# Kernel tuning notes

Measured on AMD Instinct MI355X. Metric: run time of the kernel, lower is better.

Reference implementation:

```python
import jax, jax.numpy as jnp
import numpy as np

B, S, H = 32, 2048, 1024

def setup_inputs() -> dict:
    key = jax.random.key(0)
    ks = jax.random.split(key, 8)
    scale = 1.0 / np.sqrt(H)
    return {
        "query": jax.random.normal(ks[0], (B, H), jnp.float32),
        "keys": jax.random.normal(ks[1], (B, S, H), jnp.float32),
        "Wa_w": jax.random.uniform(ks[2], (H, H), jnp.float32, -scale, scale),
        "Wa_b": jax.random.uniform(ks[3], (H,), jnp.float32, -scale, scale),
        "Ua_w": jax.random.uniform(ks[4], (H, H), jnp.float32, -scale, scale),
        "Ua_b": jax.random.uniform(ks[5], (H,), jnp.float32, -scale, scale),
        "Va_w": jax.random.uniform(ks[6], (1, H), jnp.float32, -scale, scale),
        "Va_b": jax.random.uniform(ks[7], (1,), jnp.float32, -scale, scale),
    }

def reference(query, keys, Wa_w, Wa_b, Ua_w, Ua_b, Va_w, Va_b):
    # q_proj: [B, H]; k_proj: [B, S, H]  (torch Linear: x @ W^T + b)
    q_proj = query @ Wa_w.T + Wa_b
    k_proj = jnp.einsum("bsh,gh->bsg", keys, Ua_w) + Ua_b
    # scores: [B, S, 1] via thin Va projection of tanh-combined features
    scores = jnp.tanh(q_proj[:, None, :] + k_proj) @ Va_w.T + Va_b
    weights = jax.nn.softmax(scores, axis=1)            # [B, S, 1]
    context = jnp.einsum("bsx,bsh->bxh", weights, keys)  # [B, 1, H]
    return context, weights[:, :, 0]
```

## Files before the change

### kernel.cpp

```cpp
#include <hip/hip_runtime.h>
#include <hip/hip_bf16.h>
#include <stdint.h>

#define B_ 32
#define S_ 2048
#define H_ 1024

typedef __attribute__((ext_vector_type(8))) short short8;
typedef __attribute__((ext_vector_type(4))) float floatx4;

__device__ inline unsigned short f32_bf16(float f) {
    union { float f; unsigned u; } v; v.f = f;
    unsigned u = v.u;
    u += 0x7fff + ((u >> 16) & 1);
    return (unsigned short)(u >> 16);
}
__device__ inline unsigned pack_bf2(float a, float b) {
    return (unsigned)f32_bf16(a) | ((unsigned)f32_bf16(b) << 16);
}
__device__ inline float bf_lo(unsigned u) { union { unsigned u; float f; } v; v.u = u << 16; return v.f; }
__device__ inline float bf_hi(unsigned u) { union { unsigned u; float f; } v; v.u = u & 0xffff0000u; return v.f; }

__device__ inline float tanh_fast(float x) {
    float e = __expf(2.0f * x);
    return 1.0f - 2.0f / (e + 1.0f);
}

__device__ inline void gld16(const void* g, void* l) {
    __builtin_amdgcn_global_load_lds(
        (const __attribute__((address_space(1))) unsigned int*)g,
        (__attribute__((address_space(3))) unsigned int*)l, 16, 0, 0);
}

#define KCVT_BLOCKS 32768
#define UACVT_BLOCKS 512
#define QP_BLOCKS 64
__global__ void k_prep(const float* __restrict__ keys, unsigned short* __restrict__ keysbf,
                       const float* __restrict__ ua, unsigned short* __restrict__ uab,
                       const float* __restrict__ query, const float* __restrict__ Wa_w,
                       const float* __restrict__ Wa_b, const float* __restrict__ Ua_b,
                       float* __restrict__ qsum) {
    int blk = blockIdx.x, t = threadIdx.x;
    if (blk < KCVT_BLOCKS + UACVT_BLOCKS) {
        const float* src; unsigned short* dst; size_t base;
        if (blk < KCVT_BLOCKS) { src = keys; dst = keysbf; base = (size_t)blk * 2048; }
        else { src = ua; dst = uab; base = (size_t)(blk - KCVT_BLOCKS) * 2048; }
        float4 v0 = *(const float4*)(src + base + t * 4);
        float4 v1 = *(const float4*)(src + base + 1024 + t * 4);
        *(uint2*)(dst + base + t * 4)        = make_uint2(pack_bf2(v0.x, v0.y), pack_bf2(v0.z, v0.w));
        *(uint2*)(dst + base + 1024 + t * 4) = make_uint2(pack_bf2(v1.x, v1.y), pack_bf2(v1.z, v1.w));
    } else {
        __shared__ float qs_l[32][68];
        int g0 = (blk - KCVT_BLOCKS - UACVT_BLOCKS) * 16;
        int r = t >> 4, l = t & 15;
        int g = g0 + r;
        float acc[32];
#pragma unroll
        for (int b = 0; b < 32; ++b) acc[b] = 0.0f;
        int sb = t >> 3, sc = (t & 7) * 8;
        for (int hc = 0; hc < 16; ++hc) {
            __syncthreads();
            float4 v0 = *(const float4*)(query + (size_t)sb * H_ + hc * 64 + sc);
            float4 v1 = *(const float4*)(query + (size_t)sb * H_ + hc * 64 + sc + 4);
            *(float4*)&qs_l[sb][sc]     = v0;
            *(float4*)&qs_l[sb][sc + 4] = v1;
            __syncthreads();
            float4 w = *(const float4*)(Wa_w + (size_t)g * H_ + hc * 64 + l * 4);
#pragma unroll
            for (int b = 0; b < 32; ++b) {
                float4 q4 = *(const float4*)&qs_l[b][l * 4];
                acc[b] += w.x * q4.x + w.y * q4.y + w.z * q4.z + w.w * q4.w;
            }
        }
#pragma unroll
        for (int b = 0; b < 32; ++b) {
            float a = acc[b];
            a += __shfl_xor(a, 1); a += __shfl_xor(a, 2);
            a += __shfl_xor(a, 4); a += __shfl_xor(a, 8);
            acc[b] = a;
        }
        if (l == 0) {
            float bias = Wa_b[g] + Ua_b[g];
#pragma unroll
            for (int b = 0; b < 32; ++b) qsum[b * H_ + g] = acc[b] + bias;
        }
    }
}

#define BM 128
#define BN 128
#define BK 64

__global__ __launch_bounds__(256, 4) void k_scores(
    const unsigned short* __restrict__ keysbf, const unsigned short* __restrict__ uab,
    const float* __restrict__ qsum, const float* __restrict__ va,
    float* __restrict__ scores_p)
{
    __shared__ unsigned short Al[BM * BK];
    __shared__ unsigned short Bl[BN * BK];

    int bx = blockIdx.x;
    int x  = bx & 7;
    int i  = bx >> 3;
    int tile_m = x * 64 + (i >> 3);
    int nc     = i & 7;
    int m_base = tile_m * BM;
    int b      = m_base >> 11;
    int g0     = nc * BN;

    int tid = threadIdx.x;
    int wid = tid >> 6, lane = tid & 63;
    int wm = wid >> 1, wn = wid & 1;
    int q = lane >> 4, cn = lane & 15;

    int rl8 = lane >> 3;
    int gcg = (lane & 7) ^ rl8;
    const unsigned short* pA[4];
    const unsigned short* pB[4];
    unsigned short* lA[4];
    unsigned short* lB[4];
#pragma unroll
    for (int j = 0; j < 4; ++j) {
        int row = wid * 32 + j * 8 + rl8;
        pA[j] = keysbf + (size_t)(m_base + row) * H_ + gcg * 8;
        pB[j] = uab    + (size_t)(g0     + row) * H_ + gcg * 8;
        lA[j] = &Al[(wid * 32 + j * 8) * BK];
        lB[j] = &Bl[(wid * 32 + j * 8) * BK];
    }

    int aoff[2][4], boff[2][4];
#pragma unroll
    for (int kk = 0; kk < 2; ++kk)
#pragma unroll
        for (int ii = 0; ii < 4; ++ii) {
            int r  = wm * 64 + ii * 16 + cn;
            aoff[kk][ii] = r * BK + ((kk * 4 + q) ^ (r & 7)) * 8;
            int rb = wn * 64 + ii * 16 + cn;
            boff[kk][ii] = rb * BK + ((kk * 4 + q) ^ (rb & 7)) * 8;
        }

    floatx4 acc[4][4];
#pragma unroll
    for (int ii = 0; ii < 4; ++ii)
#pragma unroll
        for (int jj = 0; jj < 4; ++jj)
            acc[ii][jj] = (floatx4)(0.0f);

    for (int kc = 0; kc < H_ / BK; ++kc) {
        __syncthreads();
        int ko = kc * BK;
#pragma unroll
        for (int j = 0; j < 4; ++j) {
            gld16(pA[j] + ko, lA[j]);
            gld16(pB[j] + ko, lB[j]);
        }
        __syncthreads();
#pragma unroll
        for (int kk = 0; kk < 2; ++kk) {
            short8 af[4], bf[4];
#pragma unroll
            for (int ii = 0; ii < 4; ++ii) af[ii] = *(const short8*)&Al[aoff[kk][ii]];
#pragma unroll
            for (int jj = 0; jj < 4; ++jj) bf[jj] = *(const short8*)&Bl[boff[kk][jj]];
#pragma unroll
            for (int ii = 0; ii < 4; ++ii)
#pragma unroll
                for (int jj = 0; jj < 4; ++jj)
                    acc[ii][jj] = __builtin_amdgcn_mfma_f32_16x16x32_bf16(
                        af[ii], bf[jj], acc[ii][jj], 0, 0, 0);
        }
    }

    float qs[4], vw[4];
#pragma unroll
    for (int jj = 0; jj < 4; ++jj) {
        int g = g0 + wn * 64 + jj * 16 + cn;
        qs[jj] = qsum[b * H_ + g];
        vw[jj] = va[g];
    }
    float* slab = scores_p + (size_t)nc * (B_ * S_) + b * S_;
#pragma unroll
    for (int ii = 0; ii < 4; ++ii) {
        float rs[4] = {0.f, 0.f, 0.f, 0.f};
#pragma unroll
        for (int jj = 0; jj < 4; ++jj) {
#pragma unroll
            for (int r = 0; r < 4; ++r)
                rs[r] += vw[jj] * tanh_fast(qs[jj] + acc[ii][jj][r]);
        }
#pragma unroll
        for (int r = 0; r < 4; ++r) {
            for (int mm = 1; mm < 16; mm <<= 1)
                rs[r] += __shfl_xor(rs[r], mm);
        }
        if (cn == 0) {
            int msrow = (m_base & (S_ - 1)) + wm * 64 + ii * 16 + q * 4;
            float* sp = slab + (size_t)wn * (8 * B_ * S_) + msrow;
            sp[0] = rs[0]; sp[1] = rs[1]; sp[2] = rs[2]; sp[3] = rs[3];
        }
    }
}

__global__ void k_softmax(const float* __restrict__ scores_p, float* __restrict__ weights) {
    int b = blockIdx.x;
    int t = threadIdx.x;
    __shared__ float red[4];
    float v[8];
    float mx = -1e30f;
#pragma unroll
    for (int k = 0; k < 8; ++k) {
        int idx = b * S_ + t + k * 256;
        float s = 0.0f;
#pragma unroll
        for (int p = 0; p < 16; ++p) s += scores_p[(size_t)p * (B_ * S_) + idx];
        v[k] = s; mx = fmaxf(mx, s);
    }
    for (int mm = 1; mm < 64; mm <<= 1) mx = fmaxf(mx, __shfl_xor(mx, mm));
    if ((t & 63) == 0) red[t >> 6] = mx;
    __syncthreads();
    mx = fmaxf(fmaxf(red[0], red[1]), fmaxf(red[2], red[3]));
    float sum = 0.0f;
#pragma unroll
    for (int k = 0; k < 8; ++k) { v[k] = __expf(v[k] - mx); sum += v[k]; }
    for (int mm = 1; mm < 64; mm <<= 1) sum += __shfl_xor(sum, mm);
    __syncthreads();
    if ((t & 63) == 0) red[t >> 6] = sum;
    __syncthreads();
    sum = red[0] + red[1] + red[2] + red[3];
    float inv = 1.0f / sum;
#pragma unroll
    for (int k = 0; k < 8; ++k) weights[b * S_ + t + k * 256] = v[k] * inv;
}

__global__ void k_ctx1(const unsigned short* __restrict__ keysbf,
                       const float* __restrict__ weights, float* __restrict__ partial) {
    int blk = blockIdx.x;
    int b = blk >> 5, sc = blk & 31;
    int t = threadIdx.x;
    __shared__ float wl[64];
    if (t < 64) wl[t] = weights[b * S_ + sc * 64 + t];
    __syncthreads();
    const uint4* kp = (const uint4*)(keysbf + (size_t)(b * S_ + sc * 64) * H_);
    int col = t & 127;
    int rp  = t >> 7;
    float a0=0,a1=0,a2=0,a3=0,a4=0,a5=0,a6=0,a7=0;
#pragma unroll 8
    for (int s = rp; s < 64; s += 2) {
        uint4 v = kp[(size_t)s * 128 + col];
        float w = wl[s];
        a0 += w * bf_lo(v.x); a1 += w * bf_hi(v.x);
        a2 += w * bf_lo(v.y); a3 += w * bf_hi(v.y);
        a4 += w * bf_lo(v.z); a5 += w * bf_hi(v.z);
        a6 += w * bf_lo(v.w); a7 += w * bf_hi(v.w);
    }
    float* pp = partial + (size_t)(b * 64 + sc * 2 + rp) * H_ + col * 8;
    float4 o0 = {a0, a1, a2, a3}, o1 = {a4, a5, a6, a7};
    *(float4*)pp = o0;
    *(float4*)(pp + 4) = o1;
}

__global__ void k_ctx2(const float* __restrict__ partial, float* __restrict__ ctx) {
    int b = blockIdx.x;
    int t = threadIdx.x;
    float4 a = {0.f, 0.f, 0.f, 0.f};
#pragma unroll 8
    for (int j = 0; j < 64; ++j) {
        float4 p = *(const float4*)(partial + (size_t)(b * 64 + j) * H_ + t * 4);
        a.x += p.x; a.y += p.y; a.z += p.z; a.w += p.w;
    }
    *(float4*)(ctx + b * H_ + t * 4) = a;
}

extern "C" void kernel_launch(void* const* d_in, const int* in_sizes, int n_in,
                              void* d_out, int out_size, void* d_ws, size_t ws_size,
                              hipStream_t stream) {
    const float* query = (const float*)d_in[0];
    const float* keys  = (const float*)d_in[1];
    const float* Wa_w  = (const float*)d_in[2];
    const float* Wa_b  = (const float*)d_in[3];
    const float* Ua_w  = (const float*)d_in[4];
    const float* Ua_b  = (const float*)d_in[5];
    const float* Va_w  = (const float*)d_in[6];

    float* out     = (float*)d_out;
    float* ctx     = out;
    float* weights = out + B_ * H_;

    char* ws = (char*)d_ws;
    unsigned short* keysbf  = (unsigned short*)ws;
    unsigned short* uab     = (unsigned short*)(ws + 134217728);
    float*          qsum    = (float*)(ws + 134217728 + 2097152);
    float*          scores_p= (float*)(ws + 134217728 + 2097152 + 131072);
    float*          partial = (float*)(ws + 134217728 + 2097152 + 131072 + 4194304);

    k_prep   <<<KCVT_BLOCKS + UACVT_BLOCKS + QP_BLOCKS, 256, 0, stream>>>(
        keys, keysbf, Ua_w, uab, query, Wa_w, Wa_b, Ua_b, qsum);
    k_scores <<<4096, 256, 0, stream>>>(keysbf, uab, qsum, Va_w, scores_p);
    k_softmax<<<B_, 256, 0, stream>>>(scores_p, weights);
    k_ctx1   <<<B_ * 32, 256, 0, stream>>>(keysbf, weights, partial);
    k_ctx2   <<<B_, 256, 0, stream>>>(partial, ctx);
}
```

Measured before the change: 592.3 us.

## Fuse keys fp32-to-bf16 conversion into the scores GEMM A-tile load

Removes the separate key-conversion pass in the prep kernel. The scores GEMM now loads fp32 keys directly, converts them to bf16 in registers and writes them into swizzled LDS. Blocks with nc==0 also write the bf16 keys to global memory for the later context kernel. This drops one full write-then-read pass over the 128MB bf16 key buffer. In exchange, the 8 column-tile blocks per row tile each re-read the fp32 keys (twice the bytes of bf16), and the A loads become synchronous register loads instead of async global_load_lds.

New measurement: 658.2 us. 11.1% more time.

```diff
diff --git a/kernel.cpp b/kernel.cpp
--- a/kernel.cpp
+++ b/kernel.cpp
@@ -32,26 +32,22 @@
         (__attribute__((address_space(3))) unsigned int*)l, 16, 0, 0);
 }
 
-#define KCVT_BLOCKS 32768
 #define UACVT_BLOCKS 512
 #define QP_BLOCKS 64
-__global__ void k_prep(const float* __restrict__ keys, unsigned short* __restrict__ keysbf,
-                       const float* __restrict__ ua, unsigned short* __restrict__ uab,
+__global__ void k_prep(const float* __restrict__ ua, unsigned short* __restrict__ uab,
                        const float* __restrict__ query, const float* __restrict__ Wa_w,
                        const float* __restrict__ Wa_b, const float* __restrict__ Ua_b,
                        float* __restrict__ qsum) {
     int blk = blockIdx.x, t = threadIdx.x;
-    if (blk < KCVT_BLOCKS + UACVT_BLOCKS) {
-        const float* src; unsigned short* dst; size_t base;
-        if (blk < KCVT_BLOCKS) { src = keys; dst = keysbf; base = (size_t)blk * 2048; }
-        else { src = ua; dst = uab; base = (size_t)(blk - KCVT_BLOCKS) * 2048; }
-        float4 v0 = *(const float4*)(src + base + t * 4);
-        float4 v1 = *(const float4*)(src + base + 1024 + t * 4);
-        *(uint2*)(dst + base + t * 4)        = make_uint2(pack_bf2(v0.x, v0.y), pack_bf2(v0.z, v0.w));
-        *(uint2*)(dst + base + 1024 + t * 4) = make_uint2(pack_bf2(v1.x, v1.y), pack_bf2(v1.z, v1.w));
+    if (blk < UACVT_BLOCKS) {
+        size_t base = (size_t)blk * 2048;
+        float4 v0 = *(const float4*)(ua + base + t * 4);
+        float4 v1 = *(const float4*)(ua + base + 1024 + t * 4);
+        *(uint2*)(uab + base + t * 4)        = make_uint2(pack_bf2(v0.x, v0.y), pack_bf2(v0.z, v0.w));
+        *(uint2*)(uab + base + 1024 + t * 4) = make_uint2(pack_bf2(v1.x, v1.y), pack_bf2(v1.z, v1.w));
     } else {
         __shared__ float qs_l[32][68];
-        int g0 = (blk - KCVT_BLOCKS - UACVT_BLOCKS) * 16;
+        int g0 = (blk - UACVT_BLOCKS) * 16;
         int r = t >> 4, l = t & 15;
         int g = g0 + r;
         float acc[32];
@@ -92,7 +88,8 @@
 #define BK 64
 
 __global__ __launch_bounds__(256, 4) void k_scores(
-    const unsigned short* __restrict__ keysbf, const unsigned short* __restrict__ uab,
+    const float* __restrict__ keys, unsigned short* __restrict__ keysbf,
+    const unsigned short* __restrict__ uab,
     const float* __restrict__ qsum, const float* __restrict__ va,
     float* __restrict__ scores_p)
 {
@@ -107,6 +104,7 @@
     int m_base = tile_m * BM;
     int b      = m_base >> 11;
     int g0     = nc * BN;
+    bool ncz   = (nc == 0);
 
     int tid = threadIdx.x;
     int wid = tid >> 6, lane = tid & 63;
@@ -114,18 +112,26 @@
     int q = lane >> 4, cn = lane & 15;
 
     int rl8 = lane >> 3;
-    int gcg = (lane & 7) ^ rl8;
-    const unsigned short* pA[4];
+    int lc8 = lane & 7;
+    int gcg = lc8 ^ rl8;
     const unsigned short* pB[4];
-    unsigned short* lA[4];
     unsigned short* lB[4];
 #pragma unroll
     for (int j = 0; j < 4; ++j) {
         int row = wid * 32 + j * 8 + rl8;
-        pA[j] = keysbf + (size_t)(m_base + row) * H_ + gcg * 8;
-        pB[j] = uab    + (size_t)(g0     + row) * H_ + gcg * 8;
-        lA[j] = &Al[(wid * 32 + j * 8) * BK];
+        pB[j] = uab + (size_t)(g0 + row) * H_ + gcg * 8;
         lB[j] = &Bl[(wid * 32 + j * 8) * BK];
+    }
+    int arow[4];
+    const float* pA[4];
+    unsigned short* wA[4];
+    unsigned short* sA[4];
+#pragma unroll
+    for (int j = 0; j < 4; ++j) {
+        arow[j] = wid * 32 + j * 8 + rl8;
+        pA[j] = keys + (size_t)(m_base + arow[j]) * H_ + lc8 * 8;
+        wA[j] = &Al[arow[j] * BK + (lc8 ^ rl8) * 8];
+        sA[j] = keysbf + (size_t)(m_base + arow[j]) * H_ + lc8 * 8;
     }
 
     int aoff[2][4], boff[2][4];
@@ -147,12 +153,22 @@
             acc[ii][jj] = (floatx4)(0.0f);
 
     for (int kc = 0; kc < H_ / BK; ++kc) {
+        int ko = kc * BK;
         __syncthreads();
-        int ko = kc * BK;
+#pragma unroll
+        for (int j = 0; j < 4; ++j)
+            gld16(pB[j] + ko, lB[j]);
 #pragma unroll
         for (int j = 0; j < 4; ++j) {
-            gld16(pA[j] + ko, lA[j]);
-            gld16(pB[j] + ko, lB[j]);
+            float4 f4a = *(const float4*)(pA[j] + ko);
+            float4 f4b = *(const float4*)(pA[j] + ko + 4);
+            uint4 pk;
+            pk.x = pack_bf2(f4a.x, f4a.y);
+            pk.y = pack_bf2(f4a.z, f4a.w);
+            pk.z = pack_bf2(f4b.x, f4b.y);
+            pk.w = pack_bf2(f4b.z, f4b.w);
+            *(uint4*)wA[j] = pk;
+            if (ncz) *(uint4*)(sA[j] + ko) = pk;
         }
         __syncthreads();
 #pragma unroll
@@ -293,9 +309,9 @@
     float*          scores_p= (float*)(ws + 134217728 + 2097152 + 131072);
     float*          partial = (float*)(ws + 134217728 + 2097152 + 131072 + 4194304);
 
-    k_prep   <<<KCVT_BLOCKS + UACVT_BLOCKS + QP_BLOCKS, 256, 0, stream>>>(
-        keys, keysbf, Ua_w, uab, query, Wa_w, Wa_b, Ua_b, qsum);
-    k_scores <<<4096, 256, 0, stream>>>(keysbf, uab, qsum, Va_w, scores_p);
+    k_prep   <<<UACVT_BLOCKS + QP_BLOCKS, 256, 0, stream>>>(
+        Ua_w, uab, query, Wa_w, Wa_b, Ua_b, qsum);
+    k_scores <<<4096, 256, 0, stream>>>(keys, keysbf, uab, qsum, Va_w, scores_p);
     k_softmax<<<B_, 256, 0, stream>>>(scores_p, weights);
     k_ctx1   <<<B_ * 32, 256, 0, stream>>>(keysbf, weights, partial);
     k_ctx2   <<<B_, 256, 0, stream>>>(partial, ctx);
```
